# Kernel tuning notes

Hardware: AMD Instinct MI355X
Metric: run time of the kernel (lower is better)

## Reference

```python
import jax, jax.numpy as jnp
import numpy as np

DIM = 2048
N_HEADS = 32
N_KV_HEADS = 8
HEAD_DIM = DIM // N_HEADS
ROPE_BASE = 10000.0
BATCH = 2
SEQ = 2048


def _rope_cos_sin(seq_len, dtype=jnp.float32):
    inv_freq = 1.0 / (ROPE_BASE ** (jnp.arange(0, HEAD_DIM, 2, dtype=jnp.float32) / HEAD_DIM))
    pos = jnp.arange(seq_len, dtype=jnp.float32)
    freqs = pos[:, None] * inv_freq[None, :]  # (seq, head_dim/2)
    return jnp.cos(freqs).astype(dtype), jnp.sin(freqs).astype(dtype)


def _apply_rope(x, cos, sin):
    # x: (b, h, s, d); cos/sin: (s, d/2). Interleaved (even/odd) RoPE.
    cos = cos[None, None, :, :]
    sin = sin[None, None, :, :]
    x_even = x[..., ::2]
    x_odd = x[..., 1::2]
    rot_even = x_even * cos - x_odd * sin
    rot_odd = x_even * sin + x_odd * cos
    out = jnp.stack((rot_even, rot_odd), axis=-1)
    return out.reshape(x.shape)


def setup_inputs() -> dict:
    key = jax.random.key(0)
    ks = jax.random.split(key, 5)
    s = 0.02
    return {
        "x": jax.random.normal(ks[0], (BATCH, SEQ, DIM), dtype=jnp.float32),
        "wq": jax.random.normal(ks[1], (DIM, N_HEADS * HEAD_DIM), dtype=jnp.float32) * s,
        "wk": jax.random.normal(ks[2], (DIM, N_KV_HEADS * HEAD_DIM), dtype=jnp.float32) * s,
        "wv": jax.random.normal(ks[3], (DIM, N_KV_HEADS * HEAD_DIM), dtype=jnp.float32) * s,
        "wo": jax.random.normal(ks[4], (DIM, DIM), dtype=jnp.float32) * s,
    }


def reference(x, wq, wk, wv, wo):
    b, s, _ = x.shape
    q = (x @ wq).reshape(b, s, N_HEADS, HEAD_DIM).transpose(0, 2, 1, 3)
    k = (x @ wk).reshape(b, s, N_KV_HEADS, HEAD_DIM).transpose(0, 2, 1, 3)
    v = (x @ wv).reshape(b, s, N_KV_HEADS, HEAD_DIM).transpose(0, 2, 1, 3)
    cos, sin = _rope_cos_sin(s, x.dtype)
    q = _apply_rope(q, cos, sin)
    k = _apply_rope(k, cos, sin)
    rep = N_HEADS // N_KV_HEADS
    if rep > 1:
        k = jnp.repeat(k, rep, axis=1)
        v = jnp.repeat(v, rep, axis=1)
    scores = jnp.einsum("bhqd,bhkd->bhqk", q, k) / (HEAD_DIM ** 0.5)
    causal = jnp.tril(jnp.ones((s, s), dtype=bool))
    scores = jnp.where(causal[None, None], scores, -jnp.inf)
    probs = jax.nn.softmax(scores, axis=-1)
    out = jnp.einsum("bhqk,bhkd->bhqd", probs, v)
    out = out.transpose(0, 2, 1, 3).reshape(b, s, DIM)
    return out @ wo
```

## Files before the change

### kernel.cpp

```cpp
#include <hip/hip_runtime.h>
#include <stdint.h>

#define DIM   2048
#define NH    32
#define NKV   8
#define HD    64
#define BATCH 2
#define SEQ   2048

typedef __attribute__((ext_vector_type(8))) short  short8;
typedef __attribute__((ext_vector_type(4))) short  short4v;
typedef __attribute__((ext_vector_type(4))) float  f32x4;

#if __has_builtin(__builtin_amdgcn_exp2f)
#define EXP2(x) __builtin_amdgcn_exp2f(x)
#else
#define EXP2(x) exp2f(x)
#endif

static __device__ __forceinline__ short f2bf(float f) {
  union { float f; uint32_t u; } v; v.f = f;
  uint32_t r = v.u + 0x7FFFu + ((v.u >> 16) & 1u);
  return (short)(r >> 16);
}

static __device__ __forceinline__ uint32_t cvtpk_bf16(float lo, float hi) {
  uint32_t r;
  asm("v_cvt_pk_bf16_f32 %0, %1, %2" : "=v"(r) : "v"(lo), "v"(hi));
  return r;
}

#define GLD16(gp, lp) __builtin_amdgcn_global_load_lds(                      \
    (__attribute__((address_space(1))) void*)(void*)(gp),                    \
    (__attribute__((address_space(3))) void*)(lp), 16, 0, 0)

#define QSCALE 0.1803368801111244f


__global__ void cvt_x_kernel(const float* __restrict__ in, short* __restrict__ out, int n4) {
  int i = blockIdx.x * blockDim.x + threadIdx.x;
  if (i < n4) {
    f32x4 v = *reinterpret_cast<const f32x4*>(in + (size_t)i * 4);
    short4v o;
    o.x = f2bf(v.x); o.y = f2bf(v.y); o.z = f2bf(v.z); o.w = f2bf(v.w);
    *reinterpret_cast<short4v*>(out + (size_t)i * 4) = o;
  }
}

__global__ void transpose_bf_kernel(const float* __restrict__ in, short* __restrict__ out,
                                    int R, int C) {
  __shared__ float t[32][33];
  int c0 = blockIdx.x * 32, r0 = blockIdx.y * 32;
  int tx = threadIdx.x, ty = threadIdx.y;
#pragma unroll
  for (int j = 0; j < 32; j += 8)
    t[ty + j][tx] = in[(size_t)(r0 + ty + j) * C + c0 + tx];
  __syncthreads();
#pragma unroll
  for (int j = 0; j < 32; j += 8)
    out[(size_t)(c0 + ty + j) * R + r0 + tx] = f2bf(t[tx][ty + j]);
}

__global__ void rope_tab_kernel(float* __restrict__ ct, float* __restrict__ st) {
  int i = blockIdx.x * blockDim.x + threadIdx.x;
  if (i < SEQ * 32) {
    int pos = i >> 5, f = i & 31;
    float inv = powf(10000.0f, -(float)f / 32.0f);
    float th = (float)pos * inv;
    ct[i] = cosf(th);
    st[i] = sinf(th);
  }
}


__device__ __forceinline__ void mfma_tile(const short* __restrict__ as_,
                                          const short* __restrict__ bs_,
                                          int wr, int wc, int lg, int lr,
                                          f32x4 (&acc)[4][4]) {
  short8 af[4], bq[4];
#pragma unroll
  for (int mt = 0; mt < 4; ++mt) {
    int row = wr * 64 + mt * 16 + lr;
    af[mt] = *(const short8*)&as_[row * 32 + ((lg ^ ((row >> 1) & 3)) << 3)];
  }
#pragma unroll
  for (int nt = 0; nt < 4; ++nt) {
    int row = wc * 64 + nt * 16 + lr;
    bq[nt] = *(const short8*)&bs_[row * 32 + ((lg ^ ((row >> 1) & 3)) << 3)];
  }
  __builtin_amdgcn_s_setprio(1);
#pragma unroll
  for (int mt = 0; mt < 4; ++mt)
#pragma unroll
    for (int nt = 0; nt < 4; ++nt)
      acc[mt][nt] = __builtin_amdgcn_mfma_f32_16x16x32_bf16(af[mt], bq[nt], acc[mt][nt], 0, 0, 0);
  __builtin_amdgcn_s_setprio(0);
}

#define STAGE4(SA, SB) do {                                                  \
    GLD16(pA0, (SA) + w * 512);  GLD16(pA1, (SA) + 2048 + w * 512);          \
    GLD16(pB0, (SB) + w * 512);  GLD16(pB1, (SB) + 2048 + w * 512);          \
    pA0 += 32; pA1 += 32; pB0 += 32; pB1 += 32; } while (0)

#define TILE(CA, CB, SA, SB, DOSTAGE, VM) do {                               \
    asm volatile("s_waitcnt vmcnt(" VM ")" ::: "memory");                    \
    __builtin_amdgcn_s_barrier();                                            \
    __builtin_amdgcn_sched_barrier(0);                                       \
    if (DOSTAGE) { STAGE4(SA, SB); }                                         \
    mfma_tile(CA, CB, wr, wc, lg, lr, acc);                                  \
  } while (0)

__device__ __forceinline__ void gemm_mainloop(const short* __restrict__ A,
                                              const short* __restrict__ Bt,
                                              int m0, int n0,
                                              short* As, short* Bs,
                                              f32x4 (&acc)[4][4]) {
  const int tid = threadIdx.x;
  const int w = tid >> 6, l = tid & 63;
  const int lg = l >> 4, lr = l & 15;
  const int wr = w >> 1, wc = w & 1;
  const int c1 = tid + 256;
  const int r0 = tid >> 2, k0 = ((tid & 3) ^ ((r0 >> 1) & 3)) << 3;
  const int r1 = c1 >> 2,  k1 = ((c1 & 3) ^ ((r1 >> 1) & 3)) << 3;
  const short* pA0 = A + (size_t)(m0 + r0) * DIM + k0;
  const short* pA1 = A + (size_t)(m0 + r1) * DIM + k1;
  const short* pB0 = Bt + (size_t)(n0 + r0) * DIM + k0;
  const short* pB1 = Bt + (size_t)(n0 + r1) * DIM + k1;
  short* A0 = As;            short* B0 = Bs;
  short* A1 = As + 4096;     short* B1 = Bs + 4096;
  short* A2 = As + 8192;     short* B2 = Bs + 8192;

  STAGE4(A0, B0);
  STAGE4(A1, B1);

  for (int it = 0; it < 20; ++it) {
    TILE(A0, B0, A2, B2, true, "4");
    TILE(A1, B1, A0, B0, true, "4");
    TILE(A2, B2, A1, B1, true, "4");
  }
  TILE(A0, B0, A2, B2, true,  "4");
  TILE(A1, B1, A0, B0, true,  "4");
  TILE(A2, B2, A0, B0, false, "4");
  TILE(A0, B0, A1, B1, false, "0");
}

__device__ __forceinline__ int2 xcd_swizzle(int nwg) {
  int id = blockIdx.y * gridDim.x + blockIdx.x;
  int swz = (id & 7) * (nwg >> 3) + (id >> 3);
  return make_int2(swz % gridDim.x, swz / gridDim.x);
}

__global__ void __launch_bounds__(256, 3)
gemm_qkv_kernel(const short* __restrict__ A,
                const short* __restrict__ wqt, const short* __restrict__ wkt,
                const short* __restrict__ wvt,
                short* __restrict__ q_ws, short* __restrict__ k_ws, short* __restrict__ v_ws,
                const float* __restrict__ ct, const float* __restrict__ st) {
  __shared__ __align__(16) short As[12288];
  __shared__ __align__(16) short Bs[12288];
  int2 bxy = xcd_swizzle(24 * 32);
  const int n0g = bxy.x * 128;
  const int m0 = bxy.y * 128;
  int mode, n0;
  const short* Bt;
  short* outp;
  if (n0g < 2048)      { mode = 1; Bt = wqt; n0 = n0g;        outp = q_ws; }
  else if (n0g < 2560) { mode = 2; Bt = wkt; n0 = n0g - 2048; outp = k_ws; }
  else                 { mode = 3; Bt = wvt; n0 = n0g - 2560; outp = v_ws; }

  f32x4 acc[4][4] = {};
  gemm_mainloop(A, Bt, m0, n0, As, Bs, acc);

  const int tid = threadIdx.x;
  const int w = tid >> 6, l = tid & 63;
  const int lg = l >> 4, lr = l & 15;
  const int wr = w >> 1, wc = w & 1;
  const int mrow0 = m0 + wr * 64;
  const int ncol0 = n0 + wc * 64;
#pragma unroll
  for (int mt = 0; mt < 4; ++mt)
#pragma unroll
    for (int nt = 0; nt < 4; ++nt)
#pragma unroll
      for (int i = 0; i < 4; ++i) {
        int m = mrow0 + mt * 16 + lg * 4 + i;
        int n = ncol0 + nt * 16 + lr;
        float v = acc[mt][nt][i];
        int b = m >> 11, s = m & (SEQ - 1);
        int h = n >> 6, d = n & 63;
        if (mode == 3) {
          outp[((size_t)(b * NKV + h) * HD + d) * SEQ + s] = f2bf(v);
        } else {
          float p = __shfl_xor(v, 1);
          float cs = ct[(s << 5) + (d >> 1)];
          float sn = st[(s << 5) + (d >> 1)];
          float r = ((d & 1) == 0) ? (v * cs - p * sn) : (p * sn + v * cs);
          if (mode == 1) {
            r *= QSCALE;
            outp[((size_t)(b * NH + h) * SEQ + s) * HD + d] = f2bf(r);
          } else {
            outp[((size_t)(b * NKV + h) * SEQ + s) * HD + d] = f2bf(r);
          }
        }
      }
}

__global__ void __launch_bounds__(256, 3)
gemm_o_kernel(const short* __restrict__ A, const short* __restrict__ Bt,
              float* __restrict__ out) {
  __shared__ __align__(16) short As[12288];
  __shared__ __align__(16) short Bs[12288];
  int2 bxy = xcd_swizzle(16 * 32);
  const int m0 = bxy.y * 128, n0 = bxy.x * 128;
  f32x4 acc[4][4] = {};
  gemm_mainloop(A, Bt, m0, n0, As, Bs, acc);
  const int tid = threadIdx.x;
  const int w = tid >> 6, l = tid & 63;
  const int lg = l >> 4, lr = l & 15;
  const int wr = w >> 1, wc = w & 1;
#pragma unroll
  for (int mt = 0; mt < 4; ++mt)
#pragma unroll
    for (int nt = 0; nt < 4; ++nt)
#pragma unroll
      for (int i = 0; i < 4; ++i) {
        int m = m0 + wr * 64 + mt * 16 + lg * 4 + i;
        int n = n0 + wc * 64 + nt * 16 + lr;
        out[(size_t)m * DIM + n] = acc[mt][nt][i];
      }
}

__global__ void __launch_bounds__(256)
attn_fwd_kernel(const short* __restrict__ Q, const short* __restrict__ K,
                const short* __restrict__ V, short* __restrict__ O) {
  __shared__ __align__(16) short Ks[2][4096];
  __shared__ __align__(16) short Vs[2][4096];
  const int tid = threadIdx.x;
  const int w = tid >> 6, l = tid & 63;
  const int lg = l >> 4, lr = l & 15;
  const int h = blockIdx.y;
  const int b = blockIdx.z;
  const int kvh = h >> 2;

  const short* kbase = K + (size_t)(b * NKV + kvh) * SEQ * HD;
  const short* vbase = V + (size_t)(b * NKV + kvh) * HD * SEQ;

  const int c1 = tid + 256;
  const int r0 = tid >> 3, e0 = ((tid & 7) ^ (r0 & 7)) << 3;
  const int r1 = c1 >> 3, e1 = ((c1 & 7) ^ (r1 & 7)) << 3;

  for (int qi = 0; qi < 2; ++qi) {
    const int qblk = (qi == 0) ? (int)blockIdx.x : (31 - (int)blockIdx.x);
    const int q0 = qblk * 64;
    const int qrow = q0 + w * 16 + lr;

    const short* qptr = Q + ((size_t)(b * NH + h) * SEQ + qrow) * HD;
    short8 qf0 = *(const short8*)(qptr + (lg << 3));
    short8 qf1 = *(const short8*)(qptr + 32 + (lg << 3));

    float m_run = -__builtin_inff(), l_run = 0.f;
    f32x4 oacc[4] = {};

    GLD16(kbase + (size_t)r0 * HD + e0, &Ks[0][w * 512]);
    GLD16(kbase + (size_t)r1 * HD + e1, &Ks[0][2048 + w * 512]);
    GLD16(vbase + (size_t)r0 * SEQ + e0, &Vs[0][w * 512]);
    GLD16(vbase + (size_t)r1 * SEQ + e1, &Vs[0][2048 + w * 512]);
    __syncthreads();

    int cur = 0;
    for (int t = 0; t <= qblk; ++t) {
      const int kv0 = t * 64;
      if (t < qblk) {
        const int kv1 = kv0 + 64;
        const int nx = cur ^ 1;
        GLD16(kbase + (size_t)(kv1 + r0) * HD + e0, &Ks[nx][w * 512]);
        GLD16(kbase + (size_t)(kv1 + r1) * HD + e1, &Ks[nx][2048 + w * 512]);
        GLD16(vbase + (size_t)r0 * SEQ + kv1 + e0, &Vs[nx][w * 512]);
        GLD16(vbase + (size_t)r1 * SEQ + kv1 + e1, &Vs[nx][2048 + w * 512]);
      }
      const short* ks = Ks[cur];
      const short* vs = Vs[cur];

      f32x4 sacc[4];
#pragma unroll
      for (int t4 = 0; t4 < 4; ++t4) {
        f32x4 z = {};
        int row = t4 * 16 + lr;
        int rx = row & 7;
        short8 a0 = *(const short8*)&ks[row * 64 + ((lg ^ rx) << 3)];
        short8 a1 = *(const short8*)&ks[row * 64 + (((4 + lg) ^ rx) << 3)];
        z = __builtin_amdgcn_mfma_f32_16x16x32_bf16(a0, qf0, z, 0, 0, 0);
        z = __builtin_amdgcn_mfma_f32_16x16x32_bf16(a1, qf1, z, 0, 0, 0);
        sacc[t4] = z;
      }

      if (t == qblk) {
#pragma unroll
        for (int t4 = 0; t4 < 4; ++t4)
#pragma unroll
          for (int i = 0; i < 4; ++i)
            if (kv0 + t4 * 16 + lg * 4 + i > qrow) sacc[t4][i] = -__builtin_inff();
      }

      float tm = fmaxf(fmaxf(fmaxf(sacc[0][0], sacc[0][1]), fmaxf(sacc[0][2], sacc[0][3])),
                       fmaxf(fmaxf(sacc[1][0], sacc[1][1]), fmaxf(sacc[1][2], sacc[1][3])));
      float tm2 = fmaxf(fmaxf(fmaxf(sacc[2][0], sacc[2][1]), fmaxf(sacc[2][2], sacc[2][3])),
                        fmaxf(fmaxf(sacc[3][0], sacc[3][1]), fmaxf(sacc[3][2], sacc[3][3])));
      tm = fmaxf(tm, tm2);
      tm = fmaxf(tm, __shfl_xor(tm, 16));
      tm = fmaxf(tm, __shfl_xor(tm, 32));

      if (!__all(tm <= m_run + 12.0f)) {
        float m_new = fmaxf(m_run, tm);
        float alpha = EXP2(m_run - m_new);
        float av0 = __shfl(alpha, (lg << 2));
        float av1 = __shfl(alpha, (lg << 2) | 1);
        float av2 = __shfl(alpha, (lg << 2) | 2);
        float av3 = __shfl(alpha, (lg << 2) | 3);
#pragma unroll
        for (int nt = 0; nt < 4; ++nt) {
          oacc[nt][0] *= av0; oacc[nt][1] *= av1;
          oacc[nt][2] *= av2; oacc[nt][3] *= av3;
        }
        l_run *= alpha;
        m_run = m_new;
      }

      float p[16];
      float lsum = 0.f;
#pragma unroll
      for (int t4 = 0; t4 < 4; ++t4)
#pragma unroll
        for (int i = 0; i < 4; ++i) {
          float e = EXP2(sacc[t4][i] - m_run);
          p[t4 * 4 + i] = e;
          lsum += e;
        }
      lsum += __shfl_xor(lsum, 16);
      lsum += __shfl_xor(lsum, 32);
      l_run += lsum;

      union { short8 s8; uint32_t u[4]; } pa0, pa1;
      pa0.u[0] = cvtpk_bf16(p[0], p[1]);
      pa0.u[1] = cvtpk_bf16(p[2], p[3]);
      pa0.u[2] = cvtpk_bf16(p[4], p[5]);
      pa0.u[3] = cvtpk_bf16(p[6], p[7]);
      pa1.u[0] = cvtpk_bf16(p[8], p[9]);
      pa1.u[1] = cvtpk_bf16(p[10], p[11]);
      pa1.u[2] = cvtpk_bf16(p[12], p[13]);
      pa1.u[3] = cvtpk_bf16(p[14], p[15]);

      const int lh = lg >> 1, sub = (lg & 1) << 2;
#pragma unroll
      for (int nt = 0; nt < 4; ++nt) {
        int row = nt * 16 + lr;
        int rx = row & 7;
#pragma unroll
        for (int ks_ = 0; ks_ < 2; ++ks_) {
          union { short8 s8; short4v h[2]; } vb;
          vb.h[0] = *(const short4v*)&vs[row * 64 + (((4 * ks_ + lh) ^ rx) << 3) + sub];
          vb.h[1] = *(const short4v*)&vs[row * 64 + (((4 * ks_ + 2 + lh) ^ rx) << 3) + sub];
          oacc[nt] = __builtin_amdgcn_mfma_f32_16x16x32_bf16(ks_ == 0 ? pa0.s8 : pa1.s8, vb.s8,
                                                             oacc[nt], 0, 0, 0);
        }
      }
      __syncthreads();
      cur ^= 1;
    }

    float lv0 = __shfl(l_run, (lg << 2));
    float lv1 = __shfl(l_run, (lg << 2) | 1);
    float lv2 = __shfl(l_run, (lg << 2) | 2);
    float lv3 = __shfl(l_run, (lg << 2) | 3);
    float linv0 = 1.f / lv0, linv1 = 1.f / lv1, linv2 = 1.f / lv2, linv3 = 1.f / lv3;
#pragma unroll
    for (int nt = 0; nt < 4; ++nt) {
      int d = nt * 16 + lr;
      int qb = q0 + w * 16 + lg * 4;
      O[(size_t)(b * SEQ + qb + 0) * DIM + h * HD + d] = f2bf(oacc[nt][0] * linv0);
      O[(size_t)(b * SEQ + qb + 1) * DIM + h * HD + d] = f2bf(oacc[nt][1] * linv1);
      O[(size_t)(b * SEQ + qb + 2) * DIM + h * HD + d] = f2bf(oacc[nt][2] * linv2);
      O[(size_t)(b * SEQ + qb + 3) * DIM + h * HD + d] = f2bf(oacc[nt][3] * linv3);
    }
  }
}


extern "C" void kernel_launch(void* const* d_in, const int* in_sizes, int n_in,
                              void* d_out, int out_size, void* d_ws, size_t ws_size,
                              hipStream_t stream) {
  const float* x  = (const float*)d_in[0];
  const float* wq = (const float*)d_in[1];
  const float* wk = (const float*)d_in[2];
  const float* wv = (const float*)d_in[3];
  const float* wo = (const float*)d_in[4];
  float* out = (float*)d_out;
  char* ws = (char*)d_ws;

  short* x_bf  = (short*)(ws + 0);
  short* attn  = (short*)(ws + 0);
  short* q_ws  = (short*)(ws + 16777216);
  short* k_ws  = (short*)(ws + 33554432);
  short* v_ws  = (short*)(ws + 37748736);
  short* wq_t  = (short*)(ws + 41943040);
  short* wo_t  = (short*)(ws + 41943040);
  short* wk_t  = (short*)(ws + 50331648);
  short* wv_t  = (short*)(ws + 52428800);
  float* ct    = (float*)(ws + 54525952);
  float* st    = (float*)(ws + 54788096);
  (void)ws_size; (void)in_sizes; (void)n_in; (void)out_size;

  dim3 tb(32, 8);
  cvt_x_kernel<<<8192, 256, 0, stream>>>(x, x_bf, 2097152);
  transpose_bf_kernel<<<dim3(64, 64), tb, 0, stream>>>(wq, wq_t, DIM, 2048);
  transpose_bf_kernel<<<dim3(16, 64), tb, 0, stream>>>(wk, wk_t, DIM, 512);
  transpose_bf_kernel<<<dim3(16, 64), tb, 0, stream>>>(wv, wv_t, DIM, 512);
  rope_tab_kernel<<<256, 256, 0, stream>>>(ct, st);

  gemm_qkv_kernel<<<dim3(24, 32), 256, 0, stream>>>(x_bf, wq_t, wk_t, wv_t,
                                                    q_ws, k_ws, v_ws, ct, st);

  attn_fwd_kernel<<<dim3(16, 32, 2), 256, 0, stream>>>(q_ws, k_ws, v_ws, attn);

  transpose_bf_kernel<<<dim3(64, 64), tb, 0, stream>>>(wo, wo_t, DIM, 2048);
  gemm_o_kernel<<<dim3(16, 32), 256, 0, stream>>>(attn, wo_t, out);
}
```

Measured before the change: 238.2 us.

## Triple-buffer attention K/V tiles and fold softmax max/sum into MFMA

The attention kernel moves from double to triple buffering of K/V tiles in LDS, with explicit vmcnt waits and a single barrier per iteration, so loads run two tiles ahead. It also hoists all K and V fragment reads ahead of the MFMAs and raises wave priority around the MFMA blocks. The running max is subtracted by seeding the QK accumulator with -m instead of a separate subtract, and the row sum comes from an MFMA against a ones vector rather than shuffle reductions. In exchange it uses more LDS and registers per block, and launch bounds are set to ask for three blocks per CU.

Result: faster. 221.6 us (-7.0%).

```diff
diff --git a/kernel.cpp b/kernel.cpp
--- a/kernel.cpp
+++ b/kernel.cpp
@@ -230,17 +230,18 @@
       }
 }
 
-__global__ void __launch_bounds__(256)
+__global__ void __launch_bounds__(256, 3)
 attn_fwd_kernel(const short* __restrict__ Q, const short* __restrict__ K,
                 const short* __restrict__ V, short* __restrict__ O) {
-  __shared__ __align__(16) short Ks[2][4096];
-  __shared__ __align__(16) short Vs[2][4096];
+  __shared__ __align__(16) short Ks[3][4096];
+  __shared__ __align__(16) short Vs[3][4096];
   const int tid = threadIdx.x;
   const int w = tid >> 6, l = tid & 63;
   const int lg = l >> 4, lr = l & 15;
   const int h = blockIdx.y;
   const int b = blockIdx.z;
   const int kvh = h >> 2;
+  const int lh = lg >> 1, sub = (lg & 1) << 2;
 
   const short* kbase = K + (size_t)(b * NKV + kvh) * SEQ * HD;
   const short* vbase = V + (size_t)(b * NKV + kvh) * HD * SEQ;
@@ -248,6 +249,16 @@
   const int c1 = tid + 256;
   const int r0 = tid >> 3, e0 = ((tid & 7) ^ (r0 & 7)) << 3;
   const int r1 = c1 >> 3, e1 = ((c1 & 7) ^ (r1 & 7)) << 3;
+
+  short8 ones;
+#pragma unroll
+  for (int i = 0; i < 8; ++i) ones[i] = (short)0x3F80;
+
+#define ASTAGE(kvt, KB, VB) do { const int kv_ = (kvt) * 64;                  \
+    GLD16(kbase + (size_t)(kv_ + r0) * HD + e0, (KB) + w * 512);              \
+    GLD16(kbase + (size_t)(kv_ + r1) * HD + e1, (KB) + 2048 + w * 512);       \
+    GLD16(vbase + (size_t)r0 * SEQ + kv_ + e0, (VB) + w * 512);               \
+    GLD16(vbase + (size_t)r1 * SEQ + kv_ + e1, (VB) + 2048 + w * 512); } while (0)
 
   for (int qi = 0; qi < 2; ++qi) {
     const int qblk = (qi == 0) ? (int)blockIdx.x : (31 - (int)blockIdx.x);
@@ -258,40 +269,58 @@
     short8 qf0 = *(const short8*)(qptr + (lg << 3));
     short8 qf1 = *(const short8*)(qptr + 32 + (lg << 3));
 
-    float m_run = -__builtin_inff(), l_run = 0.f;
+    float m_run = 0.f;
     f32x4 oacc[4] = {};
-
-    GLD16(kbase + (size_t)r0 * HD + e0, &Ks[0][w * 512]);
-    GLD16(kbase + (size_t)r1 * HD + e1, &Ks[0][2048 + w * 512]);
-    GLD16(vbase + (size_t)r0 * SEQ + e0, &Vs[0][w * 512]);
-    GLD16(vbase + (size_t)r1 * SEQ + e1, &Vs[0][2048 + w * 512]);
-    __syncthreads();
-
-    int cur = 0;
+    f32x4 lacc = {};
+
+    short* kb0 = Ks[0]; short* kb1 = Ks[1]; short* kb2 = Ks[2];
+    short* vb0 = Vs[0]; short* vb1 = Vs[1]; short* vb2 = Vs[2];
+
+    ASTAGE(0, kb0, vb0);
+    if (qblk >= 1) ASTAGE(1, kb1, vb1);
+
     for (int t = 0; t <= qblk; ++t) {
+      if (t < qblk) asm volatile("s_waitcnt vmcnt(4)" ::: "memory");
+      else          asm volatile("s_waitcnt vmcnt(0)" ::: "memory");
+      __builtin_amdgcn_s_barrier();
+      __builtin_amdgcn_sched_barrier(0);
+      if (t + 2 <= qblk) ASTAGE(t + 2, kb2, vb2);
+
+      const short* ks = kb0;
+      const short* vs = vb0;
       const int kv0 = t * 64;
-      if (t < qblk) {
-        const int kv1 = kv0 + 64;
-        const int nx = cur ^ 1;
-        GLD16(kbase + (size_t)(kv1 + r0) * HD + e0, &Ks[nx][w * 512]);
-        GLD16(kbase + (size_t)(kv1 + r1) * HD + e1, &Ks[nx][2048 + w * 512]);
-        GLD16(vbase + (size_t)r0 * SEQ + kv1 + e0, &Vs[nx][w * 512]);
-        GLD16(vbase + (size_t)r1 * SEQ + kv1 + e1, &Vs[nx][2048 + w * 512]);
-      }
-      const short* ks = Ks[cur];
-      const short* vs = Vs[cur];
+
+      short8 ka[4][2];
+#pragma unroll
+      for (int t4 = 0; t4 < 4; ++t4) {
+        int row = t4 * 16 + lr, rx = row & 7;
+        ka[t4][0] = *(const short8*)&ks[row * 64 + ((lg ^ rx) << 3)];
+        ka[t4][1] = *(const short8*)&ks[row * 64 + (((4 + lg) ^ rx) << 3)];
+      }
+      short8 vbf[4][2];
+#pragma unroll
+      for (int nt = 0; nt < 4; ++nt) {
+        int row = nt * 16 + lr, rx = row & 7;
+#pragma unroll
+        for (int ks_ = 0; ks_ < 2; ++ks_) {
+          union { short8 s8; short4v hh[2]; } u;
+          u.hh[0] = *(const short4v*)&vs[row * 64 + (((4 * ks_ + lh) ^ rx) << 3) + sub];
+          u.hh[1] = *(const short4v*)&vs[row * 64 + (((4 * ks_ + 2 + lh) ^ rx) << 3) + sub];
+          vbf[nt][ks_] = u.s8;
+        }
+      }
 
       f32x4 sacc[4];
-#pragma unroll
-      for (int t4 = 0; t4 < 4; ++t4) {
-        f32x4 z = {};
-        int row = t4 * 16 + lr;
-        int rx = row & 7;
-        short8 a0 = *(const short8*)&ks[row * 64 + ((lg ^ rx) << 3)];
-        short8 a1 = *(const short8*)&ks[row * 64 + (((4 + lg) ^ rx) << 3)];
-        z = __builtin_amdgcn_mfma_f32_16x16x32_bf16(a0, qf0, z, 0, 0, 0);
-        z = __builtin_amdgcn_mfma_f32_16x16x32_bf16(a1, qf1, z, 0, 0, 0);
-        sacc[t4] = z;
+      {
+        f32x4 seed;
+        seed[0] = -m_run; seed[1] = -m_run; seed[2] = -m_run; seed[3] = -m_run;
+        __builtin_amdgcn_s_setprio(1);
+#pragma unroll
+        for (int t4 = 0; t4 < 4; ++t4) {
+          f32x4 z = __builtin_amdgcn_mfma_f32_16x16x32_bf16(ka[t4][0], qf0, seed, 0, 0, 0);
+          sacc[t4] = __builtin_amdgcn_mfma_f32_16x16x32_bf16(ka[t4][1], qf1, z, 0, 0, 0);
+        }
+        __builtin_amdgcn_s_setprio(0);
       }
 
       if (t == qblk) {
@@ -302,17 +331,18 @@
             if (kv0 + t4 * 16 + lg * 4 + i > qrow) sacc[t4][i] = -__builtin_inff();
       }
 
-      float tm = fmaxf(fmaxf(fmaxf(sacc[0][0], sacc[0][1]), fmaxf(sacc[0][2], sacc[0][3])),
-                       fmaxf(fmaxf(sacc[1][0], sacc[1][1]), fmaxf(sacc[1][2], sacc[1][3])));
-      float tm2 = fmaxf(fmaxf(fmaxf(sacc[2][0], sacc[2][1]), fmaxf(sacc[2][2], sacc[2][3])),
-                        fmaxf(fmaxf(sacc[3][0], sacc[3][1]), fmaxf(sacc[3][2], sacc[3][3])));
-      tm = fmaxf(tm, tm2);
+      float a0 = fmaxf(fmaxf(sacc[0][0], sacc[0][1]), sacc[0][2]);
+      float a1 = fmaxf(fmaxf(sacc[0][3], sacc[1][0]), sacc[1][1]);
+      float a2 = fmaxf(fmaxf(sacc[1][2], sacc[1][3]), sacc[2][0]);
+      float a3 = fmaxf(fmaxf(sacc[2][1], sacc[2][2]), sacc[2][3]);
+      float a4 = fmaxf(fmaxf(sacc[3][0], sacc[3][1]), sacc[3][2]);
+      float tm = fmaxf(fmaxf(fmaxf(a0, a1), a2), fmaxf(fmaxf(a3, a4), sacc[3][3]));
       tm = fmaxf(tm, __shfl_xor(tm, 16));
       tm = fmaxf(tm, __shfl_xor(tm, 32));
 
-      if (!__all(tm <= m_run + 12.0f)) {
-        float m_new = fmaxf(m_run, tm);
-        float alpha = EXP2(m_run - m_new);
+      if (!__all(tm <= 12.0f)) {
+        float d = fmaxf(tm, 0.f);
+        float alpha = EXP2(-d);
         float av0 = __shfl(alpha, (lg << 2));
         float av1 = __shfl(alpha, (lg << 2) | 1);
         float av2 = __shfl(alpha, (lg << 2) | 2);
@@ -322,57 +352,40 @@
           oacc[nt][0] *= av0; oacc[nt][1] *= av1;
           oacc[nt][2] *= av2; oacc[nt][3] *= av3;
         }
-        l_run *= alpha;
-        m_run = m_new;
-      }
-
-      float p[16];
-      float lsum = 0.f;
-#pragma unroll
-      for (int t4 = 0; t4 < 4; ++t4)
-#pragma unroll
-        for (int i = 0; i < 4; ++i) {
-          float e = EXP2(sacc[t4][i] - m_run);
-          p[t4 * 4 + i] = e;
-          lsum += e;
-        }
-      lsum += __shfl_xor(lsum, 16);
-      lsum += __shfl_xor(lsum, 32);
-      l_run += lsum;
+        lacc[0] *= av0; lacc[1] *= av1; lacc[2] *= av2; lacc[3] *= av3;
+        m_run += d;
+#pragma unroll
+        for (int t4 = 0; t4 < 4; ++t4)
+#pragma unroll
+          for (int i = 0; i < 4; ++i) sacc[t4][i] -= d;
+      }
 
       union { short8 s8; uint32_t u[4]; } pa0, pa1;
-      pa0.u[0] = cvtpk_bf16(p[0], p[1]);
-      pa0.u[1] = cvtpk_bf16(p[2], p[3]);
-      pa0.u[2] = cvtpk_bf16(p[4], p[5]);
-      pa0.u[3] = cvtpk_bf16(p[6], p[7]);
-      pa1.u[0] = cvtpk_bf16(p[8], p[9]);
-      pa1.u[1] = cvtpk_bf16(p[10], p[11]);
-      pa1.u[2] = cvtpk_bf16(p[12], p[13]);
-      pa1.u[3] = cvtpk_bf16(p[14], p[15]);
-
-      const int lh = lg >> 1, sub = (lg & 1) << 2;
+      pa0.u[0] = cvtpk_bf16(EXP2(sacc[0][0]), EXP2(sacc[0][1]));
+      pa0.u[1] = cvtpk_bf16(EXP2(sacc[0][2]), EXP2(sacc[0][3]));
+      pa0.u[2] = cvtpk_bf16(EXP2(sacc[1][0]), EXP2(sacc[1][1]));
+      pa0.u[3] = cvtpk_bf16(EXP2(sacc[1][2]), EXP2(sacc[1][3]));
+      pa1.u[0] = cvtpk_bf16(EXP2(sacc[2][0]), EXP2(sacc[2][1]));
+      pa1.u[1] = cvtpk_bf16(EXP2(sacc[2][2]), EXP2(sacc[2][3]));
+      pa1.u[2] = cvtpk_bf16(EXP2(sacc[3][0]), EXP2(sacc[3][1]));
+      pa1.u[3] = cvtpk_bf16(EXP2(sacc[3][2]), EXP2(sacc[3][3]));
+
+      __builtin_amdgcn_s_setprio(1);
 #pragma unroll
       for (int nt = 0; nt < 4; ++nt) {
-        int row = nt * 16 + lr;
-        int rx = row & 7;
-#pragma unroll
-        for (int ks_ = 0; ks_ < 2; ++ks_) {
-          union { short8 s8; short4v h[2]; } vb;
-          vb.h[0] = *(const short4v*)&vs[row * 64 + (((4 * ks_ + lh) ^ rx) << 3) + sub];
-          vb.h[1] = *(const short4v*)&vs[row * 64 + (((4 * ks_ + 2 + lh) ^ rx) << 3) + sub];
-          oacc[nt] = __builtin_amdgcn_mfma_f32_16x16x32_bf16(ks_ == 0 ? pa0.s8 : pa1.s8, vb.s8,
-                                                             oacc[nt], 0, 0, 0);
-        }
-      }
-      __syncthreads();
-      cur ^= 1;
+        oacc[nt] = __builtin_amdgcn_mfma_f32_16x16x32_bf16(pa0.s8, vbf[nt][0], oacc[nt], 0, 0, 0);
+        oacc[nt] = __builtin_amdgcn_mfma_f32_16x16x32_bf16(pa1.s8, vbf[nt][1], oacc[nt], 0, 0, 0);
+      }
+      lacc = __builtin_amdgcn_mfma_f32_16x16x32_bf16(pa0.s8, ones, lacc, 0, 0, 0);
+      lacc = __builtin_amdgcn_mfma_f32_16x16x32_bf16(pa1.s8, ones, lacc, 0, 0, 0);
+      __builtin_amdgcn_s_setprio(0);
+
+      short* tk = kb0; kb0 = kb1; kb1 = kb2; kb2 = tk;
+      short* tv = vb0; vb0 = vb1; vb1 = vb2; vb2 = tv;
     }
 
-    float lv0 = __shfl(l_run, (lg << 2));
-    float lv1 = __shfl(l_run, (lg << 2) | 1);
-    float lv2 = __shfl(l_run, (lg << 2) | 2);
-    float lv3 = __shfl(l_run, (lg << 2) | 3);
-    float linv0 = 1.f / lv0, linv1 = 1.f / lv1, linv2 = 1.f / lv2, linv3 = 1.f / lv3;
+    float linv0 = 1.f / lacc[0], linv1 = 1.f / lacc[1];
+    float linv2 = 1.f / lacc[2], linv3 = 1.f / lacc[3];
 #pragma unroll
     for (int nt = 0; nt < 4; ++nt) {
       int d = nt * 16 + lr;
@@ -382,7 +395,9 @@
       O[(size_t)(b * SEQ + qb + 2) * DIM + h * HD + d] = f2bf(oacc[nt][2] * linv2);
       O[(size_t)(b * SEQ + qb + 3) * DIM + h * HD + d] = f2bf(oacc[nt][3] * linv3);
     }
-  }
+    __syncthreads();
+  }
+#undef ASTAGE
 }
 
 
```
